# Kernel tuning notes

Measured on AMD Instinct MI355X. Metric: run time of the kernel, lower is better.

## Reference

```python
import jax, jax.numpy as jnp
import numpy as np


def setup_inputs() -> dict:
    key = jax.random.key(0)
    k1, k2, k3 = jax.random.split(key, 3)
    B, S, IN, OUT = 2, 4096, 4096, 11008
    # int8 activations and weights, matching torch.randint(-127, 127, ...)
    x = jax.random.randint(k1, (B, S, IN), -127, 127, dtype=jnp.int8)
    weight = jax.random.randint(k2, (OUT, IN), -127, 127, dtype=jnp.int8)
    bias = jax.random.normal(k3, (1, OUT), dtype=jnp.float32)
    alpha = jnp.array(1e-3, dtype=jnp.float32)  # input_scale * weight_scale
    return {"x": x, "weight": weight, "bias": bias, "alpha": alpha}


def reference(x, weight, bias, alpha):
    # y = SiLU(alpha * (x_i8 @ W_i8^T) + beta * bias), beta = 1.0, output fp32
    x_shape = x.shape
    x2d = x.reshape(-1, x_shape[-1])  # [N, in]
    acc = jnp.matmul(x2d.astype(jnp.int32), weight.T.astype(jnp.int32))  # [N, out] int32
    y = alpha * acc.astype(jnp.float32) + bias  # fused dequant + bias epilogue
    y = y * jax.nn.sigmoid(y)  # SiLU
    return y.reshape(*x_shape[:-1], -1)
```

## Files before the change

### kernel.cpp

```cpp
#include <hip/hip_runtime.h>
#include <stdint.h>

#define BM 256
#define BN 256
#define BKB 128

typedef __attribute__((ext_vector_type(4)))  int i32x4;
typedef __attribute__((ext_vector_type(16))) int i32x16;

__device__ __forceinline__ void async16(const void* g, void* l) {
    __builtin_amdgcn_global_load_lds(
        (const __attribute__((address_space(1))) unsigned int*)g,
        (__attribute__((address_space(3))) unsigned int*)l,
        16 , 0 , 0 );
}

__global__ void pack_both(const int4* __restrict__ sx, int* __restrict__ dx, int nx4,
                          const int4* __restrict__ sw, int* __restrict__ dw, int nw4) {
    int idx    = blockIdx.x * blockDim.x + threadIdx.x;
    int stride = gridDim.x * blockDim.x;
    for (int i = idx; i < nx4; i += stride) {
        int4 a = sx[i];
        dx[i] = (a.x & 0xFF) | ((a.y & 0xFF) << 8) | ((a.z & 0xFF) << 16) | (a.w << 24);
    }
    for (int i = idx; i < nw4; i += stride) {
        int4 a = sw[i];
        dw[i] = (a.x & 0xFF) | ((a.y & 0xFF) << 8) | ((a.z & 0xFF) << 16) | (a.w << 24);
    }
}

__global__ __launch_bounds__(512, 2) void w8a8_silu_kernel(
    const int8_t* __restrict__ x, const int8_t* __restrict__ w,
    const float* __restrict__ bias, const float* __restrict__ alpha_p,
    float* __restrict__ out, int M, int N, int K, int nbn)
{
    __shared__ int8_t lds_a[2][BM * BKB];
    __shared__ int8_t lds_b[2][BN * BKB];

    const int tid  = threadIdx.x;
    const int lane = tid & 63;
    const int wave = tid >> 6;

    int bid = blockIdx.x;
    const int nwg = gridDim.x;
    if ((nwg & 7) == 0) bid = (bid & 7) * (nwg >> 3) + (bid >> 3);
    const int bm = bid / nbn;
    const int bn = bid - bm * nbn;

    const int srow  = tid >> 3;
    const int skoff = (((tid & 7) ^ ((tid >> 3) & 7)) << 4);
    const int8_t* gA = x + ((size_t)bm * BM + srow) * K + skoff;
    const int8_t* gB = w + ((size_t)bn * BN + srow) * K + skoff;
    const int ldst = tid * 16;

    const int wr  = (wave >> 2) * 128;
    const int wc  = (wave & 3) * 64;
    const int l31 = lane & 31;
    const int q2  = lane >> 5;
    const int xr  = l31 & 7;

    i32x16 acc[4][2] = {};

    const int NT = K / BKB;

#define STAGE_A(T, BUF) { const size_t kk = (size_t)(T) * BKB;                       \
    _Pragma("unroll") for (int j = 0; j < 4; ++j)                                     \
        async16(gA + (size_t)(j * 64) * K + kk, &lds_a[BUF][j * 8192 + ldst]); }
#define STAGE_B(T, BUF) { const size_t kk = (size_t)(T) * BKB;                       \
    _Pragma("unroll") for (int j = 0; j < 4; ++j)                                     \
        async16(gB + (size_t)(j * 64) * K + kk, &lds_b[BUF][j * 8192 + ldst]); }

    STAGE_A(0, 0);
    STAGE_B(0, 0);
    asm volatile("s_waitcnt vmcnt(0)" ::: "memory");
    __builtin_amdgcn_s_barrier();

    for (int t = 0; t < NT; ++t) {
        const int cb = t & 1;
        const int8_t* la = lds_a[cb];
        const int8_t* lb = lds_b[cb];
        const bool pf = (t + 1 < NT);

#pragma unroll
        for (int ks = 0; ks < 4; ++ks) {
            i32x4 af[4], bf[2];
            const int ck = ((ks * 2 + q2) ^ xr) << 4;
#pragma unroll
            for (int f = 0; f < 4; ++f)
                af[f] = *(const i32x4*)(la + ((wr + f * 32 + l31) << 7) + ck);
#pragma unroll
            for (int f = 0; f < 2; ++f)
                bf[f] = *(const i32x4*)(lb + ((wc + f * 32 + l31) << 7) + ck);

            if (ks == 0 && pf) STAGE_A(t + 1, cb ^ 1);
            if (ks == 1 && pf) STAGE_B(t + 1, cb ^ 1);

            __builtin_amdgcn_s_barrier();
            asm volatile("s_waitcnt lgkmcnt(0)" ::: "memory");
            __builtin_amdgcn_sched_barrier(0);
            __builtin_amdgcn_s_setprio(1);
#pragma unroll
            for (int mf = 0; mf < 4; ++mf)
#pragma unroll
                for (int nf = 0; nf < 2; ++nf)
                    acc[mf][nf] = __builtin_amdgcn_mfma_i32_32x32x32_i8(
                        af[mf], bf[nf], acc[mf][nf], 0, 0, 0);
            __builtin_amdgcn_s_setprio(0);
            __builtin_amdgcn_sched_barrier(0);

            if (ks == 3) asm volatile("s_waitcnt vmcnt(0)" ::: "memory");
            __builtin_amdgcn_s_barrier();
        }
    }

    const float alpha = *alpha_p;
    const int rowb = bm * BM + wr;
    const int colb = bn * BN + wc;
#pragma unroll
    for (int nf = 0; nf < 2; ++nf) {
        const int col = colb + nf * 32 + l31;
        const float bv = bias[col];
#pragma unroll
        for (int mf = 0; mf < 4; ++mf) {
#pragma unroll
            for (int r = 0; r < 16; ++r) {
                const int row = rowb + mf * 32 + (r & 3) + ((r >> 2) << 3) + (q2 << 2);
                float y = fmaf(alpha, (float)acc[mf][nf][r], bv);
                out[(size_t)row * N + col] = y / (1.0f + __expf(-y));
            }
        }
    }
}

extern "C" void kernel_launch(void* const* d_in, const int* in_sizes, int n_in,
                              void* d_out, int out_size, void* d_ws, size_t ws_size,
                              hipStream_t stream) {
    const int*   x32   = (const int*)d_in[0];
    const int*   w32   = (const int*)d_in[1];
    const float* bias  = (const float*)d_in[2];
    const float* alpha = (const float*)d_in[3];
    float*       out   = (float*)d_out;

    const int N = in_sizes[2];
    const int K = in_sizes[1] / N;
    const int M = in_sizes[0] / K;

    int8_t* x8 = (int8_t*)d_ws;
    int8_t* w8 = x8 + (size_t)M * K;

    const int nx4 = (int)(((size_t)M * K) / 4);
    const int nw4 = (int)(((size_t)N * K) / 4);
    pack_both<<<2048, 256, 0, stream>>>((const int4*)x32, (int*)x8, nx4,
                                        (const int4*)w32, (int*)w8, nw4);

    const int nbm = M / BM, nbn = N / BN;
    w8a8_silu_kernel<<<nbm * nbn, 512, 0, stream>>>(x8, w8, bias, alpha, out, M, N, K, nbn);
}
```

Measured before the change: 960.8 us.

## Double-buffer LDS fragment reads in registers and drop per-substep barriers

Restructures the inner K loop so the next sub-step's A/B fragments are read from LDS into a second register buffer while the current MFMAs run. Both global-to-LDS prefetches for the next tile are issued at the start of the tile, and the per-substep barriers and lgkmcnt waits are replaced by a single wait and barrier per tile. This is meant to overlap LDS latency with MFMA work and cut synchronisation. In exchange it uses more registers for fragments and leaves the compiler free to schedule waits, which could cost occupancy or ordering.

```diff
diff --git a/kernel.cpp b/kernel.cpp
--- a/kernel.cpp
+++ b/kernel.cpp
@@ -70,6 +70,13 @@
     _Pragma("unroll") for (int j = 0; j < 4; ++j)                                     \
         async16(gB + (size_t)(j * 64) * K + kk, &lds_b[BUF][j * 8192 + ldst]); }
 
+#define READF(S, KS) {                                                                \
+    const int ck_ = (((KS) * 2 + q2) ^ xr) << 4;                                      \
+    _Pragma("unroll") for (int f = 0; f < 4; ++f)                                     \
+        af[S][f] = *(const i32x4*)(la + ((wr + f * 32 + l31) << 7) + ck_);            \
+    _Pragma("unroll") for (int f = 0; f < 2; ++f)                                     \
+        bf[S][f] = *(const i32x4*)(lb + ((wc + f * 32 + l31) << 7) + ck_); }
+
     STAGE_A(0, 0);
     STAGE_B(0, 0);
     asm volatile("s_waitcnt vmcnt(0)" ::: "memory");
@@ -79,38 +86,31 @@
         const int cb = t & 1;
         const int8_t* la = lds_a[cb];
         const int8_t* lb = lds_b[cb];
-        const bool pf = (t + 1 < NT);
+
+        i32x4 af[2][4], bf[2][2];
+        READF(0, 0);
+        if (t + 1 < NT) {
+            STAGE_A(t + 1, cb ^ 1);
+            STAGE_B(t + 1, cb ^ 1);
+        }
 
 #pragma unroll
         for (int ks = 0; ks < 4; ++ks) {
-            i32x4 af[4], bf[2];
-            const int ck = ((ks * 2 + q2) ^ xr) << 4;
-#pragma unroll
-            for (int f = 0; f < 4; ++f)
-                af[f] = *(const i32x4*)(la + ((wr + f * 32 + l31) << 7) + ck);
-#pragma unroll
-            for (int f = 0; f < 2; ++f)
-                bf[f] = *(const i32x4*)(lb + ((wc + f * 32 + l31) << 7) + ck);
-
-            if (ks == 0 && pf) STAGE_A(t + 1, cb ^ 1);
-            if (ks == 1 && pf) STAGE_B(t + 1, cb ^ 1);
-
-            __builtin_amdgcn_s_barrier();
-            asm volatile("s_waitcnt lgkmcnt(0)" ::: "memory");
-            __builtin_amdgcn_sched_barrier(0);
+            const int cu = ks & 1;
+            if (ks < 3) { const int nx = cu ^ 1; READF(nx, ks + 1); }
             __builtin_amdgcn_s_setprio(1);
 #pragma unroll
             for (int mf = 0; mf < 4; ++mf)
 #pragma unroll
                 for (int nf = 0; nf < 2; ++nf)
                     acc[mf][nf] = __builtin_amdgcn_mfma_i32_32x32x32_i8(
-                        af[mf], bf[nf], acc[mf][nf], 0, 0, 0);
+                        af[cu][mf], bf[cu][nf], acc[mf][nf], 0, 0, 0);
             __builtin_amdgcn_s_setprio(0);
-            __builtin_amdgcn_sched_barrier(0);
+        }
 
-            if (ks == 3) asm volatile("s_waitcnt vmcnt(0)" ::: "memory");
-            __builtin_amdgcn_s_barrier();
-        }
+        asm volatile("s_waitcnt vmcnt(0)" ::: "memory");
+        __builtin_amdgcn_s_barrier();
+        __builtin_amdgcn_sched_barrier(0);
     }
 
     const float alpha = *alpha_p;
```

Result: no change. 949.1 us (-1.2%).
